# Performance work log

Hardware: AMD Instinct MI355X
Metric: run time of the kernel (lower is better)

The kernel has to match this reference:

```python
import jax, jax.numpy as jnp
import numpy as np


def setup_inputs() -> dict:
    key = jax.random.key(0)
    ks = jax.random.split(key, 14)
    B, Ld, Lq, D = 64, 512, 128, 512
    d_node = jax.random.normal(ks[0], (B, Ld, D), jnp.float32)
    q_node = jax.random.normal(ks[1], (B, Lq, D), jnp.float32)
    qq_graph = jax.random.randint(ks[2], (B, Lq, Lq), 0, 2, jnp.int32)
    dq_graph = jax.random.randint(ks[3], (B, Ld, Lq), 0, 2, jnp.int32)
    dd_graph = jax.random.randint(ks[4], (B, Ld, Ld), 0, 2, jnp.int32)
    qd_graph = jax.random.randint(ks[5], (B, Lq, Ld), 0, 2, jnp.int32)
    s = 0.02
    W_nw = jax.random.normal(ks[6], (1, D), jnp.float32) * s
    b_nw = jnp.zeros((1,), jnp.float32)
    W_self = jax.random.normal(ks[7], (D, D), jnp.float32) * s
    b_self = jnp.zeros((D,), jnp.float32)
    W_dd = jax.random.normal(ks[8], (D, D), jnp.float32) * s
    W_qq = jax.random.normal(ks[9], (D, D), jnp.float32) * s
    W_dq = jax.random.normal(ks[10], (D, D), jnp.float32) * s
    W_qd = jax.random.normal(ks[11], (D, D), jnp.float32) * s
    return {"d_node": d_node, "q_node": q_node, "qq_graph": qq_graph,
            "dq_graph": dq_graph, "dd_graph": dd_graph, "qd_graph": qd_graph,
            "W_nw": W_nw, "b_nw": b_nw, "W_self": W_self, "b_self": b_self,
            "W_dd": W_dd, "W_qq": W_qq, "W_dq": W_dq, "W_qd": W_qd,
            "iteration_steps": 2}


def reference(d_node, q_node, qq_graph, dq_graph, dd_graph, qd_graph,
              W_nw, b_nw, W_self, b_self, W_dd, W_qq, W_dq, W_qd,
              iteration_steps):
    dd = dd_graph.astype(jnp.float32)
    dq = dq_graph.astype(jnp.float32)
    qq = qq_graph.astype(jnp.float32)
    qd = qd_graph.astype(jnp.float32)

    # neighbor counts, clamped to 1 where a node has no neighbors
    d_nb = dd.sum(-1) + dq.sum(-1)              # [B, Ld]
    d_nb = jnp.where(d_nb >= 1.0, d_nb, 1.0)
    q_nb = qq.sum(-1) + qd.sum(-1)              # [B, Lq]
    q_nb = jnp.where(q_nb >= 1.0, q_nb, 1.0)

    all_d_w, all_q_w = [], []
    for _ in range(iteration_steps):
        d_w = jax.nn.sigmoid(jnp.einsum('bld,od->blo', d_node, W_nw) + b_nw)[..., 0]  # [B, Ld]
        q_w = jax.nn.sigmoid(jnp.einsum('bld,od->blo', q_node, W_nw) + b_nw)[..., 0]  # [B, Lq]
        all_d_w.append(d_w)
        all_q_w.append(q_w)

        self_d = jnp.einsum('bld,od->blo', d_node, W_self) + b_self
        self_q = jnp.einsum('bld,od->blo', q_node, W_self) + b_self
        dd_info = jnp.einsum('bld,od->blo', d_node, W_dd)
        qd_info = jnp.einsum('bld,od->blo', d_node, W_qd)
        qq_info = jnp.einsum('bld,od->blo', q_node, W_qq)
        dq_info = jnp.einsum('bld,od->blo', q_node, W_dq)

        # masked weights: graph is 0/1, so replace_masked_values(., graph, 0) == graph * weight
        dd_msg = jnp.einsum('bij,bjd->bid', dd * d_w[:, None, :], dd_info)  # [B,Ld,D]
        qd_msg = jnp.einsum('bij,bjd->bid', qd * d_w[:, None, :], qd_info)  # [B,Lq,D]
        qq_msg = jnp.einsum('bij,bjd->bid', qq * q_w[:, None, :], qq_info)  # [B,Lq,D]
        dq_msg = jnp.einsum('bij,bjd->bid', dq * q_w[:, None, :], dq_info)  # [B,Ld,D]

        agg_q = (qq_msg + qd_msg) / q_nb[..., None]
        agg_d = (dd_msg + dq_msg) / d_nb[..., None]
        d_node = jax.nn.relu(self_d + agg_d)
        q_node = jax.nn.relu(self_q + agg_q)

    all_d_w = jnp.stack(all_d_w, axis=1)  # [B, steps, Ld]
    all_q_w = jnp.stack(all_q_w, axis=1)  # [B, steps, Lq]
    return (d_node, q_node, all_d_w, all_q_w)
```

## Files before the change

kernel.cpp:

```cpp
#include <hip/hip_runtime.h>
#include <cstdint>
#include <cstddef>

typedef _Float16 h16;
typedef __attribute__((ext_vector_type(8))) _Float16 h16x8;
typedef __attribute__((ext_vector_type(4))) _Float16 h16x4;
typedef __attribute__((ext_vector_type(4))) float f32x4;

constexpr int B_ = 64, LD = 512, LQ = 128, DIM = 512, STEPS = 2;
constexpr int MD = B_ * LD;
constexpr int MQ = B_ * LQ;
constexpr int KST = LD + LQ;
constexpr int KAGG = KST + DIM;

struct Src {
  const h16* p0; int s0; long bstr0;
  const h16* p1; int s1; long bstr1;
  int ksplit;
};

template <class Epi>
__device__ __forceinline__ void gemm_body(int b, long tileM, long tileN,
                                          Src sa, Src sb, int K,
                                          const Epi& epi, h16* lds) {
  const int tid = threadIdx.x;
  const int lane = tid & 63;
  const int wv = tid >> 6;
  const int wm = (wv >> 1) * 64, wn = (wv & 1) * 64;
  const int quad = lane >> 4, l16 = lane & 15;
  const int r = tid >> 2;
  const int kq = tid & 3;

  const h16* pa0 = sa.p0 + (size_t)b * sa.bstr0 + (tileM + r) * (long)sa.s0 + kq * 8;
  const h16* pa0h = pa0 + 64L * sa.s0;
  const h16* pa1 = sa.p1 + (size_t)b * sa.bstr1 + (tileM + r) * (long)sa.s1 + kq * 8 - sa.ksplit;
  const h16* pa1h = pa1 + 64L * sa.s1;
  const h16* pb0 = sb.p0 + (size_t)b * sb.bstr0 + (tileN + r) * (long)sb.s0 + kq * 8;
  const h16* pb0h = pb0 + 64L * sb.s0;
  const h16* pb1 = sb.p1 + (size_t)b * sb.bstr1 + (tileN + r) * (long)sb.s1 + kq * 8 - sb.ksplit;
  const h16* pb1h = pb1 + 64L * sb.s1;

  const int pw = (kq * 128 + (r ^ (2 * kq))) * 8;
  h16* const dA = &lds[pw];
  h16* const dB = &lds[4096 + pw];

  const h16* fA[4];
  const h16* fB[4];
#pragma unroll
  for (int t = 0; t < 4; t++) {
    const int rowA = wm + t * 16 + l16;
    const int rowB = wn + t * 16 + l16;
    fA[t] = &lds[(quad * 128 + (rowA ^ (2 * quad))) * 8];
    fB[t] = &lds[4096 + (quad * 128 + (rowB ^ (2 * quad))) * 8];
  }

  f32x4 acc[4][4] = {};
  const int T = K >> 5;

  h16x8 s0[4], s1[4];
  auto loadInto = [&](h16x8* s, int t) {
    const int k0 = t * 32;
    const bool fa = k0 < sa.ksplit;
    s[0] = *(const h16x8*)((fa ? pa0 : pa1) + k0);
    s[1] = *(const h16x8*)((fa ? pa0h : pa1h) + k0);
    const bool fb = k0 < sb.ksplit;
    s[2] = *(const h16x8*)((fb ? pb0 : pb1) + k0);
    s[3] = *(const h16x8*)((fb ? pb0h : pb1h) + k0);
  };
  auto writeLDS = [&](const h16x8* s, int c) {
    const int o = c * 8192;
    *(h16x8*)(dA + o) = s[0];
    *(h16x8*)(dA + o + 512) = s[1];
    *(h16x8*)(dB + o) = s[2];
    *(h16x8*)(dB + o + 512) = s[3];
  };
  auto mfma16 = [&](const int off) {
    h16x8 af[4], bf[4];
#pragma unroll
    for (int i = 0; i < 4; i++) {
      af[i] = *(const h16x8*)(fA[i] + off);
      bf[i] = *(const h16x8*)(fB[i] + off);
    }
#pragma unroll
    for (int i = 0; i < 4; i++)
#pragma unroll
      for (int j = 0; j < 4; j++)
        acc[i][j] = __builtin_amdgcn_mfma_f32_16x16x32_f16(af[i], bf[j], acc[i][j], 0, 0, 0);
  };

  loadInto(s0, 0);
  writeLDS(s0, 0);
  loadInto(s0, 1);
  if (2 < T) loadInto(s1, 2);

  for (int t = 0; t < T; t += 2) {
    __syncthreads();
    {
      h16x8 af[4], bf[4];
#pragma unroll
      for (int i = 0; i < 4; i++) { af[i] = *(const h16x8*)fA[i]; bf[i] = *(const h16x8*)fB[i]; }
      writeLDS(s0, 1);
      if (t + 3 < T) loadInto(s0, t + 3);
#pragma unroll
      for (int i = 0; i < 4; i++)
#pragma unroll
        for (int j = 0; j < 4; j++)
          acc[i][j] = __builtin_amdgcn_mfma_f32_16x16x32_f16(af[i], bf[j], acc[i][j], 0, 0, 0);
    }
    __syncthreads();
    {
      h16x8 af[4], bf[4];
#pragma unroll
      for (int i = 0; i < 4; i++) { af[i] = *(const h16x8*)(fA[i] + 8192); bf[i] = *(const h16x8*)(fB[i] + 8192); }
      if (t + 2 < T) writeLDS(s1, 0);
      if (t + 4 < T) loadInto(s1, t + 4);
#pragma unroll
      for (int i = 0; i < 4; i++)
#pragma unroll
        for (int j = 0; j < 4; j++)
          acc[i][j] = __builtin_amdgcn_mfma_f32_16x16x32_f16(af[i], bf[j], acc[i][j], 0, 0, 0);
    }
  }

#pragma unroll
  for (int i = 0; i < 4; i++) {
#pragma unroll
    for (int j = 0; j < 4; j++) {
      const int gm0 = (int)tileM + wm + i * 16 + quad * 4;
      const int gn  = (int)tileN + wn + j * 16 + l16;
#pragma unroll
      for (int rr = 0; rr < 4; rr++) epi(b, gm0 + rr, gn, acc[i][j][rr]);
    }
  }
}

struct EpiDense {
  const float* w;
  h16* stackA;
  h16* stackB;
  int lnShift;
  int offA, offB;
  __device__ void operator()(int, int gm, int gn, float v) const {
    const int b = gn >> lnShift, l = gn & ((1 << lnShift) - 1);
    const h16 sv = (h16)(w[gn] * v);
    if (gm < 512)
      stackA[((size_t)b * 512 + gm) * 640 + offA + l] = sv;
    else
      stackB[((size_t)b * 512 + (gm - 512)) * 640 + offB + l] = sv;
  }
};
struct EpiAgg {
  const float* bias;
  float* out;
  h16* nodeNext;
  int rowsPerB;
  __device__ void operator()(int b, int gm, int gn, float v) const {
    const size_t row = (size_t)b * rowsPerB + gm;
    const float val = fmaxf(v + bias[gn], 0.f);
    if (out) out[row * 512 + gn] = val;
    nodeNext[row * 512 + gn] = (h16)val;
  }
};

__global__ __launch_bounds__(256) void k_dense(Src saD, Src sbD, EpiDense epiD,
                                               Src saQ, Src sbQ, EpiDense epiQ) {
  __shared__ __align__(16) h16 lds[2 * 2 * 4096];
  const int g = blockIdx.x;
  const int x = g / 320;
  const int yy = g % 320;
  if (yy < 256)
    gemm_body(0, (long)x * 128, (long)yy * 128, saD, sbD, 512, epiD, lds);
  else
    gemm_body(0, (long)x * 128, (long)(yy - 256) * 128, saQ, sbQ, 512, epiQ, lds);
}

__global__ __launch_bounds__(256) void k_agg(Src saD, Src sbD, EpiAgg epiD,
                                             Src saQ, Src sbQ, EpiAgg epiQ) {
  __shared__ __align__(16) h16 lds[2 * 2 * 4096];
  const int g = blockIdx.x;
  const int b = g & 63;
  const int inner = g >> 6;
  if (inner < 16)
    gemm_body(b, (long)(inner >> 2) * 128, (long)(inner & 3) * 128, saD, sbD, KAGG, epiD, lds);
  else
    gemm_body(b, 0L, (long)(inner - 16) * 128, saQ, sbQ, KAGG, epiQ, lds);
}

__global__ __launch_bounds__(256) void k_convert(const float* __restrict__ dn,
                                                 const float* __restrict__ qn,
                                                 h16* __restrict__ dnb,
                                                 h16* __restrict__ qnb) {
  const size_t i4 = ((size_t)blockIdx.x * 256 + threadIdx.x) * 4;
  constexpr size_t TD = (size_t)MD * DIM;
  const float* src; h16* dst; size_t idx;
  if (i4 < TD) { src = dn; dst = dnb; idx = i4; }
  else         { src = qn; dst = qnb; idx = i4 - TD; }
  const float4 v = *(const float4*)&src[idx];
  h16x4 o; o.x = (h16)v.x; o.y = (h16)v.y; o.z = (h16)v.z; o.w = (h16)v.w;
  *(h16x4*)&dst[idx] = o;
}

__global__ __launch_bounds__(256) void k_wcat(const float* __restrict__ Wself,
                                              const float* __restrict__ Wdd,
                                              const float* __restrict__ Wqd,
                                              const float* __restrict__ Wqq,
                                              const float* __restrict__ Wdq,
                                              h16* __restrict__ catD,
                                              h16* __restrict__ catQ) {
  const int i = blockIdx.x * 256 + threadIdx.x;
  float vD, vQ;
  if (i < 512 * 512)       { vD = Wself[i];            vQ = vD; }
  else if (i < 1024 * 512) { vD = Wdd[i - 512 * 512];  vQ = Wqq[i - 512 * 512]; }
  else                     { vD = Wqd[i - 1024 * 512]; vQ = Wdq[i - 1024 * 512]; }
  catD[i] = (h16)vD; catQ[i] = (h16)vQ;
}

__global__ __launch_bounds__(256) void k_maskD(const int* __restrict__ dd,
                                               const int* __restrict__ dq,
                                               h16* __restrict__ maskD) {
  const int row = blockIdx.x * 4 + (threadIdx.x >> 6);
  const int lane = threadIdx.x & 63;
  const int* pdd = dd + (size_t)row * 512;
  const int* pdq = dq + (size_t)row * 128;
  h16* pm = maskD + (size_t)row * 640;
  float vals[10];
  float s = 0.f;
#pragma unroll
  for (int t = 0; t < 10; t++) {
    const int j = lane + t * 64;
    const float v = (float)((j < 512) ? pdd[j] : pdq[j - 512]);
    vals[t] = v; s += v;
  }
  for (int m = 32; m; m >>= 1) s += __shfl_xor(s, m);
  const float inv = 1.f / fmaxf(s, 1.f);
#pragma unroll
  for (int t = 0; t < 10; t++) pm[lane + t * 64] = (h16)(vals[t] * inv);
}

__global__ __launch_bounds__(256) void k_maskQ(const int* __restrict__ qq,
                                               const int* __restrict__ qd,
                                               h16* __restrict__ maskQ) {
  const int row = blockIdx.x * 4 + (threadIdx.x >> 6);
  const int lane = threadIdx.x & 63;
  const int* pqq = qq + (size_t)row * 128;
  const int* pqd = qd + (size_t)row * 512;
  h16* pm = maskQ + (size_t)row * 640;
  float vals[10];
  float s = 0.f;
#pragma unroll
  for (int t = 0; t < 10; t++) {
    const int j = lane + t * 64;
    const float v = (float)((j < 128) ? pqq[j] : pqd[j - 128]);
    vals[t] = v; s += v;
  }
  for (int m = 32; m; m >>= 1) s += __shfl_xor(s, m);
  const float inv = 1.f / fmaxf(s, 1.f);
#pragma unroll
  for (int t = 0; t < 10; t++) pm[lane + t * 64] = (h16)(vals[t] * inv);
}

__global__ __launch_bounds__(256) void k_w(const h16* __restrict__ dnb,
                                           const h16* __restrict__ qnb,
                                           const float* __restrict__ Wnw,
                                           const float* __restrict__ bnw,
                                           float* __restrict__ d_w,
                                           float* __restrict__ q_w,
                                           float* __restrict__ adw,
                                           float* __restrict__ aqw, int it) {
  const int row = blockIdx.x * 4 + (threadIdx.x >> 6);
  const int lane = threadIdx.x & 63;
  const bool isD = row < MD;
  const h16* node = isD ? dnb + (size_t)row * 512 : qnb + (size_t)(row - MD) * 512;
  const h16x8 v = *(const h16x8*)&node[lane * 8];
  const float4 w0 = *(const float4*)&Wnw[lane * 8];
  const float4 w1 = *(const float4*)&Wnw[lane * 8 + 4];
  float s = (float)v[0] * w0.x + (float)v[1] * w0.y + (float)v[2] * w0.z +
            (float)v[3] * w0.w + (float)v[4] * w1.x + (float)v[5] * w1.y +
            (float)v[6] * w1.z + (float)v[7] * w1.w;
  for (int m = 32; m; m >>= 1) s += __shfl_xor(s, m);
  if (lane == 0) {
    const float w = 1.f / (1.f + expf(-(s + bnw[0])));
    if (isD) {
      d_w[row] = w;
      adw[((size_t)(row >> 9) * STEPS + it) * 512 + (row & 511)] = w;
    } else {
      const int rq = row - MD;
      q_w[rq] = w;
      aqw[((size_t)(rq >> 7) * STEPS + it) * 128 + (rq & 127)] = w;
    }
  }
}

extern "C" void kernel_launch(void* const* d_in, const int* in_sizes, int n_in,
                              void* d_out, int out_size, void* d_ws, size_t ws_size,
                              hipStream_t stream) {
  (void)in_sizes; (void)n_in; (void)out_size; (void)ws_size;

  const float* d_node = (const float*)d_in[0];
  const float* q_node = (const float*)d_in[1];
  const int*   qq     = (const int*)d_in[2];
  const int*   dq     = (const int*)d_in[3];
  const int*   dd     = (const int*)d_in[4];
  const int*   qd     = (const int*)d_in[5];
  const float* W_nw   = (const float*)d_in[6];
  const float* b_nw   = (const float*)d_in[7];
  const float* W_self = (const float*)d_in[8];
  const float* b_self = (const float*)d_in[9];
  const float* W_dd   = (const float*)d_in[10];
  const float* W_qq   = (const float*)d_in[11];
  const float* W_dq   = (const float*)d_in[12];
  const float* W_qd   = (const float*)d_in[13];

  float* outd = (float*)d_out;
  float* outq = outd + (size_t)MD * DIM;
  float* adw  = outq + (size_t)MQ * DIM;
  float* aqw  = adw + (size_t)B_ * STEPS * LD;

  char* p = (char*)d_ws;
  auto alloc = [&](size_t bytes) { char* r = p; p += (bytes + 255) & ~(size_t)255; return r; };
  h16* dnode[2], *qnode[2];
  dnode[0] = (h16*)alloc((size_t)MD * DIM * 2);
  dnode[1] = (h16*)alloc((size_t)MD * DIM * 2);
  qnode[0] = (h16*)alloc((size_t)MQ * DIM * 2);
  qnode[1] = (h16*)alloc((size_t)MQ * DIM * 2);
  h16* catD    = (h16*)alloc((size_t)1536 * 512 * 2);
  h16* catQ    = (h16*)alloc((size_t)1536 * 512 * 2);
  h16* maskD   = (h16*)alloc((size_t)B_ * LD * KST * 2);
  h16* maskQ   = (h16*)alloc((size_t)B_ * LQ * KST * 2);
  h16* stackDT = (h16*)alloc((size_t)B_ * 512 * KST * 2);
  h16* stackQT = (h16*)alloc((size_t)B_ * 512 * KST * 2);
  float* d_wb  = (float*)alloc((size_t)MD * 4);
  float* q_wb  = (float*)alloc((size_t)MQ * 4);

  k_convert<<<dim3((MD * DIM + MQ * DIM) / 4 / 256), 256, 0, stream>>>(d_node, q_node, dnode[0], qnode[0]);
  k_wcat<<<dim3(1536 * 512 / 256), 256, 0, stream>>>(W_self, W_dd, W_qd, W_qq, W_dq, catD, catQ);
  k_maskD<<<dim3(MD / 4), 256, 0, stream>>>(dd, dq, maskD);
  k_maskQ<<<dim3(MQ / 4), 256, 0, stream>>>(qq, qd, maskQ);

  for (int it = 0; it < STEPS; it++) {
    const bool last = (it == STEPS - 1);
    h16* ncur_d = dnode[it & 1];
    h16* nnext_d = dnode[(it & 1) ^ 1];
    h16* ncur_q = qnode[it & 1];
    h16* nnext_q = qnode[(it & 1) ^ 1];

    k_w<<<dim3((MD + MQ) / 4), 256, 0, stream>>>(ncur_d, ncur_q, W_nw, b_nw, d_wb, q_wb, adw, aqw, it);

    {
      Src saD{catD + 512 * 512, 512, 0, catD + 512 * 512, 512, 0, 512};
      Src sbD{ncur_d, 512, 0, ncur_d, 512, 0, 512};
      Src saQ{catQ + 512 * 512, 512, 0, catQ + 512 * 512, 512, 0, 512};
      Src sbQ{ncur_q, 512, 0, ncur_q, 512, 0, 512};
      k_dense<<<dim3(2560), 256, 0, stream>>>(
          saD, sbD, EpiDense{d_wb, stackDT, stackQT, 9, 0, 128},
          saQ, sbQ, EpiDense{q_wb, stackQT, stackDT, 7, 0, 512});
    }
    {
      Src saD{maskD, 640, (long)LD * KST, ncur_d, 512, (long)LD * DIM, KST};
      Src sbD{stackDT, 640, (long)512 * KST, catD, 512, 0, KST};
      Src saQ{maskQ, 640, (long)LQ * KST, ncur_q, 512, (long)LQ * DIM, KST};
      Src sbQ{stackQT, 640, (long)512 * KST, catQ, 512, 0, KST};
      k_agg<<<dim3(1280), 256, 0, stream>>>(
          saD, sbD, EpiAgg{b_self, last ? outd : nullptr, nnext_d, 512},
          saQ, sbQ, EpiAgg{b_self, last ? outq : nullptr, nnext_q, 128});
    }
  }
}
```

Baseline: 627.1 us.

## Stage GEMM tiles via direct global-to-LDS async loads with swizzled layout

Replaces register-staged global loads followed by LDS stores with the global_load_lds builtin. Tiles now go straight into LDS, and the bank swizzle moves to the global-address side through an XOR on the k-quarter index. The pipeline shrinks to a plain double buffer that prefetches one tile ahead, and both GEMM kernels get a launch-bounds hint asking for 3 blocks per SM. The aim is to cut VGPR pressure and LDS write instructions so occupancy can rise. The cost is a shorter prefetch distance, and correctness relies on the barrier waiting for the async loads to land.

```diff
diff --git a/kernel.cpp b/kernel.cpp
--- a/kernel.cpp
+++ b/kernel.cpp
@@ -12,6 +12,11 @@
 constexpr int MQ = B_ * LQ;
 constexpr int KST = LD + LQ;
 constexpr int KAGG = KST + DIM;
+
+#define ASYNC16(gp, lp)                                                          \
+  __builtin_amdgcn_global_load_lds(                                              \
+      (const __attribute__((address_space(1))) unsigned int*)(gp),               \
+      (__attribute__((address_space(3))) unsigned int*)(lp), 16, 0, 0)
 
 struct Src {
   const h16* p0; int s0; long bstr0;
@@ -28,8 +33,10 @@
   const int wv = tid >> 6;
   const int wm = (wv >> 1) * 64, wn = (wv & 1) * 64;
   const int quad = lane >> 4, l16 = lane & 15;
+
   const int r = tid >> 2;
-  const int kq = tid & 3;
+  const int es = (r ^ (r >> 2)) & 3;
+  const int kq = (tid & 3) ^ es;
 
   const h16* pa0 = sa.p0 + (size_t)b * sa.bstr0 + (tileM + r) * (long)sa.s0 + kq * 8;
   const h16* pa0h = pa0 + 64L * sa.s0;
@@ -40,41 +47,34 @@
   const h16* pb1 = sb.p1 + (size_t)b * sb.bstr1 + (tileN + r) * (long)sb.s1 + kq * 8 - sb.ksplit;
   const h16* pb1h = pb1 + 64L * sb.s1;
 
-  const int pw = (kq * 128 + (r ^ (2 * kq))) * 8;
-  h16* const dA = &lds[pw];
-  h16* const dB = &lds[4096 + pw];
-
+  h16* const dA = &lds[tid * 8];
+  h16* const dB = &lds[4096 + tid * 8];
+
+  const int ef = (l16 ^ (l16 >> 2)) & 3;
   const h16* fA[4];
   const h16* fB[4];
 #pragma unroll
   for (int t = 0; t < 4; t++) {
     const int rowA = wm + t * 16 + l16;
     const int rowB = wn + t * 16 + l16;
-    fA[t] = &lds[(quad * 128 + (rowA ^ (2 * quad))) * 8];
-    fB[t] = &lds[4096 + (quad * 128 + (rowB ^ (2 * quad))) * 8];
+    fA[t] = &lds[(rowA * 4 + (quad ^ ef)) * 8];
+    fB[t] = &lds[4096 + (rowB * 4 + (quad ^ ef)) * 8];
   }
 
   f32x4 acc[4][4] = {};
   const int T = K >> 5;
 
-  h16x8 s0[4], s1[4];
-  auto loadInto = [&](h16x8* s, int t) {
+  auto dmaTile = [&](int t, int c) {
     const int k0 = t * 32;
+    const int o = c * 8192;
     const bool fa = k0 < sa.ksplit;
-    s[0] = *(const h16x8*)((fa ? pa0 : pa1) + k0);
-    s[1] = *(const h16x8*)((fa ? pa0h : pa1h) + k0);
+    ASYNC16((fa ? pa0 : pa1) + k0, dA + o);
+    ASYNC16((fa ? pa0h : pa1h) + k0, dA + o + 2048);
     const bool fb = k0 < sb.ksplit;
-    s[2] = *(const h16x8*)((fb ? pb0 : pb1) + k0);
-    s[3] = *(const h16x8*)((fb ? pb0h : pb1h) + k0);
+    ASYNC16((fb ? pb0 : pb1) + k0, dB + o);
+    ASYNC16((fb ? pb0h : pb1h) + k0, dB + o + 2048);
   };
-  auto writeLDS = [&](const h16x8* s, int c) {
-    const int o = c * 8192;
-    *(h16x8*)(dA + o) = s[0];
-    *(h16x8*)(dA + o + 512) = s[1];
-    *(h16x8*)(dB + o) = s[2];
-    *(h16x8*)(dB + o + 512) = s[3];
-  };
-  auto mfma16 = [&](const int off) {
+  auto mfma16 = [&](int off) {
     h16x8 af[4], bf[4];
 #pragma unroll
     for (int i = 0; i < 4; i++) {
@@ -88,38 +88,15 @@
         acc[i][j] = __builtin_amdgcn_mfma_f32_16x16x32_f16(af[i], bf[j], acc[i][j], 0, 0, 0);
   };
 
-  loadInto(s0, 0);
-  writeLDS(s0, 0);
-  loadInto(s0, 1);
-  if (2 < T) loadInto(s1, 2);
+  dmaTile(0, 0);
 
   for (int t = 0; t < T; t += 2) {
     __syncthreads();
-    {
-      h16x8 af[4], bf[4];
-#pragma unroll
-      for (int i = 0; i < 4; i++) { af[i] = *(const h16x8*)fA[i]; bf[i] = *(const h16x8*)fB[i]; }
-      writeLDS(s0, 1);
-      if (t + 3 < T) loadInto(s0, t + 3);
-#pragma unroll
-      for (int i = 0; i < 4; i++)
-#pragma unroll
-        for (int j = 0; j < 4; j++)
-          acc[i][j] = __builtin_amdgcn_mfma_f32_16x16x32_f16(af[i], bf[j], acc[i][j], 0, 0, 0);
-    }
+    dmaTile(t + 1, 1);
+    mfma16(0);
     __syncthreads();
-    {
-      h16x8 af[4], bf[4];
-#pragma unroll
-      for (int i = 0; i < 4; i++) { af[i] = *(const h16x8*)(fA[i] + 8192); bf[i] = *(const h16x8*)(fB[i] + 8192); }
-      if (t + 2 < T) writeLDS(s1, 0);
-      if (t + 4 < T) loadInto(s1, t + 4);
-#pragma unroll
-      for (int i = 0; i < 4; i++)
-#pragma unroll
-        for (int j = 0; j < 4; j++)
-          acc[i][j] = __builtin_amdgcn_mfma_f32_16x16x32_f16(af[i], bf[j], acc[i][j], 0, 0, 0);
-    }
+    if (t + 2 < T) dmaTile(t + 2, 0);
+    mfma16(8192);
   }
 
 #pragma unroll
@@ -162,8 +139,8 @@
   }
 };
 
-__global__ __launch_bounds__(256) void k_dense(Src saD, Src sbD, EpiDense epiD,
-                                               Src saQ, Src sbQ, EpiDense epiQ) {
+__global__ __launch_bounds__(256, 3) void k_dense(Src saD, Src sbD, EpiDense epiD,
+                                                  Src saQ, Src sbQ, EpiDense epiQ) {
   __shared__ __align__(16) h16 lds[2 * 2 * 4096];
   const int g = blockIdx.x;
   const int x = g / 320;
@@ -174,8 +151,8 @@
     gemm_body(0, (long)x * 128, (long)(yy - 256) * 128, saQ, sbQ, 512, epiQ, lds);
 }
 
-__global__ __launch_bounds__(256) void k_agg(Src saD, Src sbD, EpiAgg epiD,
-                                             Src saQ, Src sbQ, EpiAgg epiQ) {
+__global__ __launch_bounds__(256, 3) void k_agg(Src saD, Src sbD, EpiAgg epiD,
+                                                Src saQ, Src sbQ, EpiAgg epiQ) {
   __shared__ __align__(16) h16 lds[2 * 2 * 4096];
   const int g = blockIdx.x;
   const int b = g & 63;
```

After: 568.9 us. 9.3% less time.
